# Kernel optimization log

Measured on AMD Instinct MI355X. Metric: run time of the kernel, lower is better.

The kernel has to match this reference:

```python
import jax, jax.numpy as jnp
import numpy as np

B = 131072
INPUT_DIM = 256
HIDDEN_DIM = 512
LATENT_DIM = 64
K = 5


def setup_inputs() -> dict:
    key = jax.random.key(0)
    ks = jax.random.split(key, 12)

    def lin(k, out_d, in_d):
        kw, kb = jax.random.split(k)
        bound = 1.0 / np.sqrt(in_d)
        W = jax.random.uniform(kw, (out_d, in_d), jnp.float32, -bound, bound)
        b = jax.random.uniform(kb, (out_d,), jnp.float32, -bound, bound)
        return W, b

    x = jax.random.normal(ks[0], (B, INPUT_DIM), jnp.float32)
    W_eh, b_eh = lin(ks[1], HIDDEN_DIM, INPUT_DIM)      # encoder hidden Linear
    W_eo, b_eo = lin(ks[2], LATENT_DIM, HIDDEN_DIM)     # encoder out Linear
    W_dh, b_dh = lin(ks[3], HIDDEN_DIM, LATENT_DIM)     # decoder hidden Linear
    W_do, b_do = lin(ks[4], INPUT_DIM, HIDDEN_DIM)      # decoder out Linear
    pre_bias = jnp.zeros((INPUT_DIM,), jnp.float32)
    latent_bias = jax.random.uniform(ks[5], (LATENT_DIM,), jnp.float32, -0.1, 0.1)
    decoder_bias = jnp.zeros((INPUT_DIM,), jnp.float32)
    return {
        "x": x, "pre_bias": pre_bias,
        "W_eh": W_eh, "b_eh": b_eh, "W_eo": W_eo, "b_eo": b_eo,
        "latent_bias": latent_bias,
        "W_dh": W_dh, "b_dh": b_dh, "W_do": W_do, "b_do": b_do,
        "decoder_bias": decoder_bias,
    }


def reference(x, pre_bias, W_eh, b_eh, W_eo, b_eo, latent_bias,
              W_dh, b_dh, W_do, b_do, decoder_bias):
    # encode: pre-bias centering -> hidden MLP (relu) -> latent pre-activation
    xc = x - pre_bias                                   # [B, input_dim]
    h = jax.nn.relu(xc @ W_eh.T + b_eh)                 # [B, hidden]
    pre_act = h @ W_eo.T + b_eo + latent_bias           # [B, latent]

    # TopK activation: keep raw top-k values (no ReLU), zero the rest
    vals, idx = jax.lax.top_k(pre_act, K)               # [B, K]
    rows = jnp.arange(pre_act.shape[0])[:, None]        # [B, 1]
    sparse_latent = jnp.zeros_like(pre_act).at[rows, idx].set(vals)
    mask = jnp.zeros(pre_act.shape, jnp.bool_).at[rows, idx].set(True)

    # decode: hidden MLP (relu) -> output linear + decoder_bias + pre_bias
    hd = jax.nn.relu(sparse_latent @ W_dh.T + b_dh)     # [B, hidden]
    recon = hd @ W_do.T + b_do + decoder_bias + pre_bias  # [B, input_dim]

    sparsity = mask.astype(jnp.float32).mean()
    return recon, sparse_latent, pre_act, mask, sparsity
```

## Files before the change

kernel.cpp:

```cpp
#include <hip/hip_runtime.h>
#include <hip/hip_bf16.h>
#include <stdint.h>

#define B_TOT 131072
#define GAP_TAU 2.5e-4f

typedef short v8s __attribute__((ext_vector_type(8)));
typedef float v4f __attribute__((ext_vector_type(4)));

__device__ __forceinline__ unsigned short f2bf(float f) {
    union { __hip_bfloat16 b; unsigned short s; } v;
    v.b = __float2bfloat16(f);
    return v.s;
}
__device__ __forceinline__ float bf2f(unsigned short s) {
    union { unsigned u; float f; } v; v.u = ((unsigned)s) << 16;
    return v.f;
}
__device__ __forceinline__ unsigned pack2(float lo, float hi) {
    return (unsigned)f2bf(lo) | ((unsigned)f2bf(hi) << 16);
}

__global__ void k_prep(const float* __restrict__ W_dh,
                       const float* __restrict__ b_do,
                       const float* __restrict__ dec_b,
                       const float* __restrict__ pre_bias,
                       const float* __restrict__ W_do,
                       const float* __restrict__ W_eh,
                       const float* __restrict__ W_eo,
                       unsigned short* __restrict__ WdhB,
                       float* __restrict__ bias3,
                       unsigned short* __restrict__ Wdo_frag,
                       unsigned short* __restrict__ WehHi,
                       unsigned short* __restrict__ WehLo,
                       unsigned short* __restrict__ WeoHi,
                       unsigned short* __restrict__ WeoLo,
                       float* __restrict__ WehT,
                       float* __restrict__ WeoT,
                       float* __restrict__ spars_out,
                       int* __restrict__ fcount)
{
    int t = blockIdx.x * blockDim.x + threadIdx.x;
    int nthr = gridDim.x * blockDim.x;
    for (int g = t; g < 32 * 2 * 64; g += nthr) {
        int lane = g & 63;
        int rem = g >> 6;
        int kc = rem & 1, ht = rem >> 1;
        int h = ht * 16 + (lane & 15);
        int l = kc * 32 + (lane >> 4) * 8;
        const float* src = &W_dh[(size_t)h * 64 + l];
        unsigned short* dst = &WdhB[(size_t)g * 8];
        #pragma unroll
        for (int i = 0; i < 8; i++) dst[i] = f2bf(src[i]);
    }
    for (int g = t; g < 16384; g += nthr) {
        int lane = g & 63;
        int q = g >> 6;
        int nt = q >> 4, kc = q & 15;
        int col = nt * 16 + (lane & 15);
        int kbase = kc * 32 + (lane >> 4) * 8;
        const float* src = &W_do[(size_t)col * 512 + kbase];
        unsigned short* dst = &Wdo_frag[(size_t)g * 8];
        #pragma unroll
        for (int i = 0; i < 8; i++) dst[i] = f2bf(src[i]);
    }
    for (int g = t; g < 32 * 8 * 64; g += nthr) {
        int lane = g & 63;
        int rem = g >> 6;
        int kcg = rem & 7, ct = rem >> 3;
        int c = ct * 16 + (lane & 15);
        int k = kcg * 32 + (lane >> 4) * 8;
        const float* src = &W_eh[(size_t)c * 256 + k];
        #pragma unroll
        for (int i = 0; i < 8; i++) {
            unsigned short hi = f2bf(src[i]);
            WehHi[(size_t)g * 8 + i] = hi;
            WehLo[(size_t)g * 8 + i] = f2bf(src[i] - bf2f(hi));
        }
    }
    for (int g = t; g < 4 * 16 * 64; g += nthr) {
        int lane = g & 63;
        int rem = g >> 6;
        int kcg = rem & 15, lt = rem >> 4;
        int l = lt * 16 + (lane & 15);
        int k = kcg * 32 + (lane >> 4) * 8;
        const float* src = &W_eo[(size_t)l * 512 + k];
        #pragma unroll
        for (int i = 0; i < 8; i++) {
            unsigned short hi = f2bf(src[i]);
            WeoHi[(size_t)g * 8 + i] = hi;
            WeoLo[(size_t)g * 8 + i] = f2bf(src[i] - bf2f(hi));
        }
    }
    for (int i = t; i < 256 * 512; i += nthr) {
        int k = i >> 9, j = i & 511;
        WehT[i] = W_eh[(size_t)j * 256 + k];
    }
    for (int i = t; i < 512 * 64; i += nthr) {
        int k = i >> 6, l = i & 63;
        WeoT[i] = W_eo[(size_t)l * 512 + k];
    }
    if (t < 256) bias3[t] = b_do[t] + dec_b[t] + pre_bias[t];
    if (t == 0) { spars_out[0] = 5.0f / 64.0f; *fcount = 0; }
}


__global__ __launch_bounds__(512, 4)
void k_enc1(const float* __restrict__ x,
            const float* __restrict__ pre_bias,
            const unsigned short* __restrict__ WehHi,
            const unsigned short* __restrict__ WehLo,
            const float* __restrict__ b_eh,
            unsigned short* __restrict__ hHi,
            unsigned short* __restrict__ hLo)
{
    __shared__ __align__(16) unsigned short aH[64 * 256];
    __shared__ __align__(16) unsigned short aL[64 * 256];
    const int t    = threadIdx.x;
    const int lane = t & 63;
    const int w    = t >> 6;
    const int rb   = blockIdx.x * 64;

    #pragma unroll
    for (int i = 0; i < 4; i++) {
        const int f    = t + i * 512;
        const int srow = f >> 5;
        const int kc   = (f >> 2) & 7;
        const int skq  = f & 3;
        const float* xp = &x[(size_t)(rb + srow) * 256 + kc * 32 + skq * 8];
        const float* pp = &pre_bias[kc * 32 + skq * 8];
        const float4 v0 = *reinterpret_cast<const float4*>(xp);
        const float4 v1 = *reinterpret_cast<const float4*>(xp + 4);
        const float4 p0 = *reinterpret_cast<const float4*>(pp);
        const float4 p1 = *reinterpret_cast<const float4*>(pp + 4);
        float fv[8] = {v0.x - p0.x, v0.y - p0.y, v0.z - p0.z, v0.w - p0.w,
                       v1.x - p1.x, v1.y - p1.y, v1.z - p1.z, v1.w - p1.w};
        unsigned hi2[4], lo2[4];
        #pragma unroll
        for (int q = 0; q < 4; q++) {
            unsigned short h0 = f2bf(fv[q * 2]), h1 = f2bf(fv[q * 2 + 1]);
            hi2[q] = (unsigned)h0 | ((unsigned)h1 << 16);
            lo2[q] = pack2(fv[q * 2] - bf2f(h0), fv[q * 2 + 1] - bf2f(h1));
        }
        const int off = srow * 512 + ((kc * 64 + skq * 16) ^ ((srow & 7) << 4));
        *reinterpret_cast<uint4*>((char*)aH + off) = *reinterpret_cast<uint4*>(hi2);
        *reinterpret_cast<uint4*>((char*)aL + off) = *reinterpret_cast<uint4*>(lo2);
    }
    __syncthreads();

    const int rt0 = rb >> 4;
    const int q   = lane >> 4;

    #pragma unroll 1
    for (int pass = 0; pass < 2; ++pass) {
        const int ct0 = w * 4 + pass * 2;

        v4f acc[4][2];
        #pragma unroll
        for (int i = 0; i < 4; i++)
            #pragma unroll
            for (int j = 0; j < 2; j++) acc[i][j] = (v4f){0.f, 0.f, 0.f, 0.f};

        #pragma unroll 4
        for (int kc = 0; kc < 8; ++kc) {
            v8s wh[2], wl[2];
            #pragma unroll
            for (int ntl = 0; ntl < 2; ntl++) {
                const size_t idx = ((size_t)((ct0 + ntl) * 8 + kc) * 64 + lane) * 8;
                wh[ntl] = *reinterpret_cast<const v8s*>(&WehHi[idx]);
                wl[ntl] = *reinterpret_cast<const v8s*>(&WehLo[idx]);
            }
            v8s ah[4], al[4];
            #pragma unroll
            for (int mt = 0; mt < 4; mt++) {
                const int row = mt * 16 + (lane & 15);
                const int off = row * 512 + ((kc * 64 + (lane >> 4) * 16) ^ ((row & 7) << 4));
                ah[mt] = *reinterpret_cast<const v8s*>((const char*)aH + off);
                al[mt] = *reinterpret_cast<const v8s*>((const char*)aL + off);
            }
            #pragma unroll
            for (int mt = 0; mt < 4; mt++) {
                #pragma unroll
                for (int ntl = 0; ntl < 2; ntl++) {
                    acc[mt][ntl] = __builtin_amdgcn_mfma_f32_16x16x32_bf16(wh[ntl], ah[mt], acc[mt][ntl], 0, 0, 0);
                    acc[mt][ntl] = __builtin_amdgcn_mfma_f32_16x16x32_bf16(wl[ntl], ah[mt], acc[mt][ntl], 0, 0, 0);
                    acc[mt][ntl] = __builtin_amdgcn_mfma_f32_16x16x32_bf16(wh[ntl], al[mt], acc[mt][ntl], 0, 0, 0);
                }
            }
        }
        #pragma unroll
        for (int mt = 0; mt < 4; mt++) {
            #pragma unroll
            for (int ntl = 0; ntl < 2; ntl++) {
                const int ct = ct0 + ntl;
                const int c  = ct * 16 + q * 4;
                const float4 be = *reinterpret_cast<const float4*>(&b_eh[c]);
                float h0 = fmaxf(acc[mt][ntl][0] + be.x, 0.f);
                float h1 = fmaxf(acc[mt][ntl][1] + be.y, 0.f);
                float h2 = fmaxf(acc[mt][ntl][2] + be.z, 0.f);
                float h3 = fmaxf(acc[mt][ntl][3] + be.w, 0.f);
                unsigned short s0 = f2bf(h0), s1 = f2bf(h1), s2 = f2bf(h2), s3 = f2bf(h3);
                uint2 phi = { (unsigned)s0 | ((unsigned)s1 << 16), (unsigned)s2 | ((unsigned)s3 << 16) };
                uint2 plo = { pack2(h0 - bf2f(s0), h1 - bf2f(s1)),
                              pack2(h2 - bf2f(s2), h3 - bf2f(s3)) };
                const int oct = ct * 2 + (q >> 1);
                const size_t base = (((size_t)(rt0 + mt) * 64 + oct) * 16 + (lane & 15)) * 8 + (q & 1) * 4;
                *reinterpret_cast<uint2*>(&hHi[base]) = phi;
                *reinterpret_cast<uint2*>(&hLo[base]) = plo;
            }
        }
    }
}

__global__ __launch_bounds__(256, 4)
void k_enc2_topk(const unsigned short* __restrict__ hHi,
                 const unsigned short* __restrict__ hLo,
                 const unsigned short* __restrict__ WeoHi,
                 const unsigned short* __restrict__ WeoLo,
                 const float* __restrict__ b_eo,
                 const float* __restrict__ lat_b,
                 float* __restrict__ pre_out,
                 float* __restrict__ mask_out,
                 float* __restrict__ sl_out,
                 int*   __restrict__ fcount,
                 int*   __restrict__ flist)
{
    __shared__ float pa[128][68];
    __shared__ unsigned long long mbits[128];
    const int t    = threadIdx.x;
    const int lane = t & 63;
    const int w    = t >> 6;
    const int rb   = blockIdx.x * 128;
    const int rtA  = (rb >> 4) + w * 2;
    const int rtB  = rtA + 1;

    v4f acc[2][4];
    #pragma unroll
    for (int s = 0; s < 2; s++)
        #pragma unroll
        for (int i = 0; i < 4; i++) acc[s][i] = (v4f){0.f, 0.f, 0.f, 0.f};

    #pragma unroll 2
    for (int kcl = 0; kcl < 16; ++kcl) {
        const size_t baseA = ((size_t)(rtA * 64 + kcl * 4 + (lane >> 4)) * 16 + (lane & 15)) * 8;
        const size_t baseB = ((size_t)(rtB * 64 + kcl * 4 + (lane >> 4)) * 16 + (lane & 15)) * 8;
        const v8s hhA = *reinterpret_cast<const v8s*>(&hHi[baseA]);
        const v8s hlA = *reinterpret_cast<const v8s*>(&hLo[baseA]);
        const v8s hhB = *reinterpret_cast<const v8s*>(&hHi[baseB]);
        const v8s hlB = *reinterpret_cast<const v8s*>(&hLo[baseB]);
        #pragma unroll
        for (int lt = 0; lt < 4; lt++) {
            const size_t idx = ((size_t)(lt * 16 + kcl) * 64 + lane) * 8;
            const v8s wh = *reinterpret_cast<const v8s*>(&WeoHi[idx]);
            const v8s wl = *reinterpret_cast<const v8s*>(&WeoLo[idx]);
            acc[0][lt] = __builtin_amdgcn_mfma_f32_16x16x32_bf16(wh, hhA, acc[0][lt], 0, 0, 0);
            acc[0][lt] = __builtin_amdgcn_mfma_f32_16x16x32_bf16(wl, hhA, acc[0][lt], 0, 0, 0);
            acc[0][lt] = __builtin_amdgcn_mfma_f32_16x16x32_bf16(wh, hlA, acc[0][lt], 0, 0, 0);
            acc[1][lt] = __builtin_amdgcn_mfma_f32_16x16x32_bf16(wh, hhB, acc[1][lt], 0, 0, 0);
            acc[1][lt] = __builtin_amdgcn_mfma_f32_16x16x32_bf16(wl, hhB, acc[1][lt], 0, 0, 0);
            acc[1][lt] = __builtin_amdgcn_mfma_f32_16x16x32_bf16(wh, hlB, acc[1][lt], 0, 0, 0);
        }
    }
    #pragma unroll
    for (int s = 0; s < 2; s++) {
        const int row = w * 32 + s * 16 + (lane & 15);
        #pragma unroll
        for (int lt = 0; lt < 4; lt++) {
            const int l0 = lt * 16 + ((lane >> 4) << 2);
            const float4 be = *reinterpret_cast<const float4*>(&b_eo[l0]);
            const float4 lb = *reinterpret_cast<const float4*>(&lat_b[l0]);
            float4 o;
            o.x = acc[s][lt][0] + be.x + lb.x;
            o.y = acc[s][lt][1] + be.y + lb.y;
            o.z = acc[s][lt][2] + be.z + lb.z;
            o.w = acc[s][lt][3] + be.w + lb.w;
            *reinterpret_cast<float4*>(&pa[row][l0]) = o;
        }
    }
    __syncthreads();
    if (t < 128) {
        int r = t;
        unsigned long long used = 0ULL;
        float bv[5];
        #pragma unroll
        for (int p = 0; p < 5; p++) {
            float best = -3.402823466e38f; int bidx = 0;
            for (int j = 0; j < 64; j++) {
                float v = pa[r][j];
                if (!((used >> j) & 1ULL) && v > best) { best = v; bidx = j; }
            }
            used |= 1ULL << bidx;
            bv[p] = best;
        }
        mbits[r] = used;
        float v6 = -3.402823466e38f;
        for (int j = 0; j < 64; j++) {
            float v = pa[r][j];
            if (!((used >> j) & 1ULL) && v > v6) v6 = v;
        }
        if (bv[4] - v6 < GAP_TAU) {
            int slot = atomicAdd(fcount, 1);
            flist[slot] = rb + r;
        }
    }
    __syncthreads();
    {
        const int c = (t & 15) * 4;
        #pragma unroll
        for (int pass = 0; pass < 8; pass++) {
            const int row = pass * 16 + (t >> 4);
            const size_t gr = (size_t)(rb + row);
            const unsigned long long bits = mbits[row];
            const float p0 = pa[row][c + 0], p1 = pa[row][c + 1];
            const float p2 = pa[row][c + 2], p3 = pa[row][c + 3];
            const float m0 = (float)((bits >> (c + 0)) & 1ULL);
            const float m1 = (float)((bits >> (c + 1)) & 1ULL);
            const float m2 = (float)((bits >> (c + 2)) & 1ULL);
            const float m3 = (float)((bits >> (c + 3)) & 1ULL);
            float4 pv = {p0, p1, p2, p3};
            float4 mv = {m0, m1, m2, m3};
            float4 sv = {m0 * p0, m1 * p1, m2 * p2, m3 * p3};
            *reinterpret_cast<float4*>(&pre_out[gr * 64 + c])  = pv;
            *reinterpret_cast<float4*>(&mask_out[gr * 64 + c]) = mv;
            *reinterpret_cast<float4*>(&sl_out[gr * 64 + c])   = sv;
        }
    }
}

__global__ __launch_bounds__(256)
void k_repair(const float* __restrict__ x,
              const float* __restrict__ pre_bias,
              const float* __restrict__ WehT,
              const float* __restrict__ b_eh,
              const float* __restrict__ WeoT,
              const float* __restrict__ b_eo,
              const float* __restrict__ lat_b,
              const int* __restrict__ fcount,
              const int* __restrict__ flist,
              float* __restrict__ pre_out,
              float* __restrict__ mask_out,
              float* __restrict__ sl_out)
{
    __shared__ float xs[256];
    __shared__ float hs[512];
    __shared__ float part[64][4];
    const int t = threadIdx.x;
    const int n = *fcount;
    #pragma unroll 1
    for (int it = blockIdx.x; it < n; it += gridDim.x) {
        const int r = flist[it];
        xs[t] = x[(size_t)r * 256 + t] - pre_bias[t];
        __syncthreads();
        {
            float a0 = 0.f, a1 = 0.f;
            #pragma unroll 8
            for (int k = 0; k < 256; ++k) {
                const float xk = xs[k];
                a0 = fmaf(WehT[(size_t)k * 512 + t], xk, a0);
                a1 = fmaf(WehT[(size_t)k * 512 + t + 256], xk, a1);
            }
            hs[t]       = fmaxf(a0 + b_eh[t], 0.f);
            hs[t + 256] = fmaxf(a1 + b_eh[t + 256], 0.f);
        }
        __syncthreads();
        {
            const int l = t & 63, q = t >> 6;
            float acc = 0.f;
            const int k0 = q * 128;
            #pragma unroll 8
            for (int k = k0; k < k0 + 128; ++k)
                acc = fmaf(WeoT[(size_t)k * 64 + l], hs[k], acc);
            part[l][q] = acc;
        }
        __syncthreads();
        if (t < 64) {
            const float v = ((part[t][0] + part[t][1]) + (part[t][2] + part[t][3]))
                            + b_eo[t] + lat_b[t];
            unsigned long long used = 0ULL;
            #pragma unroll
            for (int p = 0; p < 5; p++) {
                float cand = ((used >> t) & 1ULL) ? -3.402823466e38f : v;
                float m = cand;
                #pragma unroll
                for (int off = 1; off < 64; off <<= 1)
                    m = fmaxf(m, __shfl_xor(m, off));
                const unsigned long long msk = __ballot(cand == m);
                const int idx = __ffsll((long long)msk) - 1;
                used |= 1ULL << idx;
            }
            const size_t gr = (size_t)r;
            const float mb = (float)((used >> t) & 1ULL);
            pre_out[gr * 64 + t]  = v;
            mask_out[gr * 64 + t] = mb;
            sl_out[gr * 64 + t]   = mb * v;
        }
        __syncthreads();
    }
}

__device__ __forceinline__ void hd_phase1(unsigned short* __restrict__ buf,
                                          const unsigned short* __restrict__ slA,
                                          const unsigned short* __restrict__ WdhB,
                                          const float* __restrict__ b_dh,
                                          int c, int w, int lane)
{
    v4f ah[2][4];
    #pragma unroll
    for (int htl = 0; htl < 2; htl++) {
        const int h0 = (c * 8 + w * 2 + htl) * 16 + ((lane >> 4) << 2);
        const float4 bd = *reinterpret_cast<const float4*>(&b_dh[h0]);
        #pragma unroll
        for (int mt = 0; mt < 4; mt++) ah[htl][mt] = (v4f){bd.x, bd.y, bd.z, bd.w};
    }
    #pragma unroll
    for (int kc = 0; kc < 2; kc++) {
        v8s sa[4];
        #pragma unroll
        for (int mt = 0; mt < 4; mt++)
            sa[mt] = *reinterpret_cast<const v8s*>(&slA[((kc * 4 + mt) * 64 + lane) * 8]);
        #pragma unroll
        for (int htl = 0; htl < 2; htl++) {
            const int ht = c * 8 + w * 2 + htl;
            const v8s wb = *reinterpret_cast<const v8s*>(&WdhB[((size_t)(ht * 2 + kc) * 64 + lane) * 8]);
            #pragma unroll
            for (int mt = 0; mt < 4; mt++)
                ah[htl][mt] = __builtin_amdgcn_mfma_f32_16x16x32_bf16(wb, sa[mt], ah[htl][mt], 0, 0, 0);
        }
    }
    #pragma unroll
    for (int htl = 0; htl < 2; htl++) {
        const int hbase = (w * 2 + htl) * 16 + ((lane >> 4) << 2);
        const int kcgl  = hbase >> 5;
        const int lp    = (((hbase & 31) >> 3) << 4) + (lane & 15);
        const int ii    = hbase & 7;
        #pragma unroll
        for (int mt = 0; mt < 4; mt++) {
            uint2 o;
            o.x = pack2(fmaxf(ah[htl][mt][0], 0.f), fmaxf(ah[htl][mt][1], 0.f));
            o.y = pack2(fmaxf(ah[htl][mt][2], 0.f), fmaxf(ah[htl][mt][3], 0.f));
            *reinterpret_cast<uint2*>(&buf[((kcgl * 4 + mt) * 64 + lp) * 8 + ii]) = o;
        }
    }
}

__global__ __launch_bounds__(256)
void k_dec(const float* __restrict__ sl,
           const float* __restrict__ b_dh,
           const unsigned short* __restrict__ WdhB,
           const unsigned short* __restrict__ Wdo_frag,
           const float* __restrict__ bias3,
           float* __restrict__ recon)
{
    __shared__ __align__(16) unsigned short slA[2 * 4 * 64 * 8];
    __shared__ __align__(16) unsigned short hdA[2][4 * 4 * 64 * 8];
    const int t    = threadIdx.x;
    const int rb   = blockIdx.x * 64;
    const int lane = t & 63;
    const int w    = t >> 6;

    {
        const int row = t >> 2;
        const int seg = (t & 3) * 16;
        const float* sp = &sl[(size_t)(rb + row) * 64 + seg];
        const int mt = row >> 4;
        #pragma unroll
        for (int q = 0; q < 4; q++) {
            const float4 v = *reinterpret_cast<const float4*>(sp + q * 4);
            const float vals[4] = {v.x, v.y, v.z, v.w};
            #pragma unroll
            for (int e = 0; e < 4; e++) {
                const int k  = seg + q * 4 + e;
                const int kc = k >> 5;
                const int lp = ((k & 31) >> 3) * 16 + (row & 15);
                slA[((kc * 4 + mt) * 64 + lp) * 8 + (k & 7)] = f2bf(vals[e]);
            }
        }
    }
    __syncthreads();

    const int g  = w >> 1;
    const int ch = w & 1;

    v4f accM[2][8];
    #pragma unroll
    for (int s = 0; s < 2; s++)
        #pragma unroll
        for (int n = 0; n < 8; n++) accM[s][n] = (v4f){0.f, 0.f, 0.f, 0.f};

    hd_phase1(hdA[0], slA, WdhB, b_dh, 0, w, lane);
    __syncthreads();

    #pragma unroll 1
    for (int c = 0; c < 4; ++c) {
        if (c < 3)
            hd_phase1(hdA[(c + 1) & 1], slA, WdhB, b_dh, c + 1, w, lane);
        const unsigned short* buf = hdA[c & 1];
        #pragma unroll
        for (int kcgl = 0; kcgl < 4; ++kcgl) {
            const int kcg = c * 4 + kcgl;
            const v8s af0 = *reinterpret_cast<const v8s*>(&buf[((kcgl * 4 + g * 2 + 0) * 64 + lane) * 8]);
            const v8s af1 = *reinterpret_cast<const v8s*>(&buf[((kcgl * 4 + g * 2 + 1) * 64 + lane) * 8]);
            #pragma unroll
            for (int ntl = 0; ntl < 8; ntl++) {
                const int ntg = ch * 8 + ntl;
                const v8s bf = *reinterpret_cast<const v8s*>(
                    Wdo_frag + ((size_t)(ntg * 16 + kcg) * 64 + lane) * 8);
                accM[0][ntl] = __builtin_amdgcn_mfma_f32_16x16x32_bf16(af0, bf, accM[0][ntl], 0, 0, 0);
                accM[1][ntl] = __builtin_amdgcn_mfma_f32_16x16x32_bf16(af1, bf, accM[1][ntl], 0, 0, 0);
            }
        }
        __syncthreads();
    }
    #pragma unroll
    for (int s = 0; s < 2; s++) {
        const int rowbase = rb + (g * 2 + s) * 16;
        #pragma unroll
        for (int ntl = 0; ntl < 8; ntl++) {
            const int col = ch * 128 + ntl * 16 + (lane & 15);
            const float bz = bias3[col];
            #pragma unroll
            for (int j = 0; j < 4; j++) {
                const size_t row = (size_t)(rowbase + (lane >> 4) * 4 + j);
                recon[row * 256 + col] = accM[s][ntl][j] + bz;
            }
        }
    }
}

extern "C" void kernel_launch(void* const* d_in, const int* in_sizes, int n_in,
                              void* d_out, int out_size, void* d_ws, size_t ws_size,
                              hipStream_t stream)
{
    const float* x        = (const float*)d_in[0];
    const float* pre_bias = (const float*)d_in[1];
    const float* W_eh     = (const float*)d_in[2];
    const float* b_eh     = (const float*)d_in[3];
    const float* W_eo     = (const float*)d_in[4];
    const float* b_eo     = (const float*)d_in[5];
    const float* lat_b    = (const float*)d_in[6];
    const float* W_dh     = (const float*)d_in[7];
    const float* b_dh     = (const float*)d_in[8];
    const float* W_do     = (const float*)d_in[9];
    const float* b_do     = (const float*)d_in[10];
    const float* dec_b    = (const float*)d_in[11];

    float* out = (float*)d_out;
    float* recon_out = out;
    float* sl_out    = out + (size_t)B_TOT * 256;
    float* pre_out   = sl_out + (size_t)B_TOT * 64;
    float* mask_out  = pre_out + (size_t)B_TOT * 64;
    float* spars_out = mask_out + (size_t)B_TOT * 64;

    char* ws = (char*)d_ws;
    unsigned short* WdhB  = (unsigned short*)ws;
    float* bias3          = (float*)(ws + 131072);
    unsigned short* WdoF  = (unsigned short*)(ws + 132096);
    unsigned short* WehHi = (unsigned short*)(ws + 394240);
    unsigned short* WehLo = (unsigned short*)(ws + 656384);
    unsigned short* WeoHi = (unsigned short*)(ws + 918528);
    unsigned short* WeoLo = (unsigned short*)(ws + 984064);
    int* fcount           = (int*)(ws + 1049600);
    int* flist            = (int*)(ws + 1049664);
    float* WehT           = (float*)(ws + 1573952);
    float* WeoT           = (float*)(ws + 2098240);
    unsigned short* hHi   = (unsigned short*)(ws + 2229312);
    unsigned short* hLo   = hHi + (size_t)B_TOT * 512;

    k_prep<<<32, 256, 0, stream>>>(W_dh, b_do, dec_b, pre_bias, W_do, W_eh, W_eo,
                                   WdhB, bias3, WdoF, WehHi, WehLo, WeoHi, WeoLo,
                                   WehT, WeoT, spars_out, fcount);

    k_enc1<<<B_TOT / 64, 512, 0, stream>>>(x, pre_bias, WehHi, WehLo, b_eh, hHi, hLo);

    k_enc2_topk<<<B_TOT / 128, 256, 0, stream>>>(hHi, hLo, WeoHi, WeoLo, b_eo, lat_b,
                                                 pre_out, mask_out, sl_out,
                                                 fcount, flist);

    k_repair<<<256, 256, 0, stream>>>(x, pre_bias, WehT, b_eh, WeoT, b_eo, lat_b,
                                      fcount, flist, pre_out, mask_out, sl_out);

    k_dec<<<B_TOT / 64, 256, 0, stream>>>(sl_out, b_dh, WdhB, WdoF, bias3, recon_out);
}
```

Before: 404.1 us.

## Fuse decoder into enc2/top-k kernel and recompute repaired rows in repair kernel

The decoder MLP is merged into the encoder-2/top-k kernel. Each block now decodes its 128 rows straight from the shared-memory pre-activations and mask bits, so the sparse latent no longer has to be read back from global memory and one kernel launch disappears. Because the repair kernel runs after decoding, it now recomputes the decoder in fp32 for the flagged rows, using a new transposed W_do copy built in prep. Shared memory per block grows and the launch bound drops to 2 blocks per CU, which may lower occupancy.

```diff
diff --git a/kernel.cpp b/kernel.cpp
--- a/kernel.cpp
+++ b/kernel.cpp
@@ -37,6 +37,7 @@
                        unsigned short* __restrict__ WeoLo,
                        float* __restrict__ WehT,
                        float* __restrict__ WeoT,
+                       float* __restrict__ WdoT,
                        float* __restrict__ spars_out,
                        int* __restrict__ fcount)
 {
@@ -99,6 +100,10 @@
     for (int i = t; i < 512 * 64; i += nthr) {
         int k = i >> 6, l = i & 63;
         WeoT[i] = W_eo[(size_t)l * 512 + k];
+    }
+    for (int i = t; i < 512 * 256; i += nthr) {
+        int h = i >> 8, c = i & 255;
+        WdoT[i] = W_do[(size_t)c * 512 + h];
     }
     if (t < 256) bias3[t] = b_do[t] + dec_b[t] + pre_bias[t];
     if (t == 0) { spars_out[0] = 5.0f / 64.0f; *fcount = 0; }
@@ -212,21 +217,73 @@
     }
 }
 
-__global__ __launch_bounds__(256, 4)
-void k_enc2_topk(const unsigned short* __restrict__ hHi,
-                 const unsigned short* __restrict__ hLo,
-                 const unsigned short* __restrict__ WeoHi,
-                 const unsigned short* __restrict__ WeoLo,
-                 const float* __restrict__ b_eo,
-                 const float* __restrict__ lat_b,
-                 float* __restrict__ pre_out,
-                 float* __restrict__ mask_out,
-                 float* __restrict__ sl_out,
-                 int*   __restrict__ fcount,
-                 int*   __restrict__ flist)
+__device__ __forceinline__ void hd_phase1(unsigned short* __restrict__ buf,
+                                          const unsigned short* __restrict__ slA,
+                                          const unsigned short* __restrict__ WdhB,
+                                          const float* __restrict__ b_dh,
+                                          int c, int w, int lane)
+{
+    v4f ah[2][4];
+    #pragma unroll
+    for (int htl = 0; htl < 2; htl++) {
+        const int h0 = (c * 8 + w * 2 + htl) * 16 + ((lane >> 4) << 2);
+        const float4 bd = *reinterpret_cast<const float4*>(&b_dh[h0]);
+        #pragma unroll
+        for (int mt = 0; mt < 4; mt++) ah[htl][mt] = (v4f){bd.x, bd.y, bd.z, bd.w};
+    }
+    #pragma unroll
+    for (int kc = 0; kc < 2; kc++) {
+        v8s sa[4];
+        #pragma unroll
+        for (int mt = 0; mt < 4; mt++)
+            sa[mt] = *reinterpret_cast<const v8s*>(&slA[((kc * 4 + mt) * 64 + lane) * 8]);
+        #pragma unroll
+        for (int htl = 0; htl < 2; htl++) {
+            const int ht = c * 8 + w * 2 + htl;
+            const v8s wb = *reinterpret_cast<const v8s*>(&WdhB[((size_t)(ht * 2 + kc) * 64 + lane) * 8]);
+            #pragma unroll
+            for (int mt = 0; mt < 4; mt++)
+                ah[htl][mt] = __builtin_amdgcn_mfma_f32_16x16x32_bf16(wb, sa[mt], ah[htl][mt], 0, 0, 0);
+        }
+    }
+    #pragma unroll
+    for (int htl = 0; htl < 2; htl++) {
+        const int hbase = (w * 2 + htl) * 16 + ((lane >> 4) << 2);
+        const int kcgl  = hbase >> 5;
+        const int lp    = (((hbase & 31) >> 3) << 4) + (lane & 15);
+        const int ii    = hbase & 7;
+        #pragma unroll
+        for (int mt = 0; mt < 4; mt++) {
+            uint2 o;
+            o.x = pack2(fmaxf(ah[htl][mt][0], 0.f), fmaxf(ah[htl][mt][1], 0.f));
+            o.y = pack2(fmaxf(ah[htl][mt][2], 0.f), fmaxf(ah[htl][mt][3], 0.f));
+            *reinterpret_cast<uint2*>(&buf[((kcgl * 4 + mt) * 64 + lp) * 8 + ii]) = o;
+        }
+    }
+}
+
+__global__ __launch_bounds__(256, 2)
+void k_enc2dec(const unsigned short* __restrict__ hHi,
+               const unsigned short* __restrict__ hLo,
+               const unsigned short* __restrict__ WeoHi,
+               const unsigned short* __restrict__ WeoLo,
+               const float* __restrict__ b_eo,
+               const float* __restrict__ lat_b,
+               float* __restrict__ pre_out,
+               float* __restrict__ mask_out,
+               float* __restrict__ sl_out,
+               int*   __restrict__ fcount,
+               int*   __restrict__ flist,
+               const float* __restrict__ b_dh,
+               const unsigned short* __restrict__ WdhB,
+               const unsigned short* __restrict__ Wdo_frag,
+               const float* __restrict__ bias3,
+               float* __restrict__ recon)
 {
     __shared__ float pa[128][68];
     __shared__ unsigned long long mbits[128];
+    __shared__ __align__(16) unsigned short slA[2 * 4 * 64 * 8];
+    __shared__ __align__(16) unsigned short hdA[2][4 * 4 * 64 * 8];
     const int t    = threadIdx.x;
     const int lane = t & 63;
     const int w    = t >> 6;
@@ -234,47 +291,49 @@
     const int rtA  = (rb >> 4) + w * 2;
     const int rtB  = rtA + 1;
 
-    v4f acc[2][4];
-    #pragma unroll
-    for (int s = 0; s < 2; s++)
-        #pragma unroll
-        for (int i = 0; i < 4; i++) acc[s][i] = (v4f){0.f, 0.f, 0.f, 0.f};
-
-    #pragma unroll 2
-    for (int kcl = 0; kcl < 16; ++kcl) {
-        const size_t baseA = ((size_t)(rtA * 64 + kcl * 4 + (lane >> 4)) * 16 + (lane & 15)) * 8;
-        const size_t baseB = ((size_t)(rtB * 64 + kcl * 4 + (lane >> 4)) * 16 + (lane & 15)) * 8;
-        const v8s hhA = *reinterpret_cast<const v8s*>(&hHi[baseA]);
-        const v8s hlA = *reinterpret_cast<const v8s*>(&hLo[baseA]);
-        const v8s hhB = *reinterpret_cast<const v8s*>(&hHi[baseB]);
-        const v8s hlB = *reinterpret_cast<const v8s*>(&hLo[baseB]);
-        #pragma unroll
-        for (int lt = 0; lt < 4; lt++) {
-            const size_t idx = ((size_t)(lt * 16 + kcl) * 64 + lane) * 8;
-            const v8s wh = *reinterpret_cast<const v8s*>(&WeoHi[idx]);
-            const v8s wl = *reinterpret_cast<const v8s*>(&WeoLo[idx]);
-            acc[0][lt] = __builtin_amdgcn_mfma_f32_16x16x32_bf16(wh, hhA, acc[0][lt], 0, 0, 0);
-            acc[0][lt] = __builtin_amdgcn_mfma_f32_16x16x32_bf16(wl, hhA, acc[0][lt], 0, 0, 0);
-            acc[0][lt] = __builtin_amdgcn_mfma_f32_16x16x32_bf16(wh, hlA, acc[0][lt], 0, 0, 0);
-            acc[1][lt] = __builtin_amdgcn_mfma_f32_16x16x32_bf16(wh, hhB, acc[1][lt], 0, 0, 0);
-            acc[1][lt] = __builtin_amdgcn_mfma_f32_16x16x32_bf16(wl, hhB, acc[1][lt], 0, 0, 0);
-            acc[1][lt] = __builtin_amdgcn_mfma_f32_16x16x32_bf16(wh, hlB, acc[1][lt], 0, 0, 0);
-        }
-    }
-    #pragma unroll
-    for (int s = 0; s < 2; s++) {
-        const int row = w * 32 + s * 16 + (lane & 15);
-        #pragma unroll
-        for (int lt = 0; lt < 4; lt++) {
-            const int l0 = lt * 16 + ((lane >> 4) << 2);
-            const float4 be = *reinterpret_cast<const float4*>(&b_eo[l0]);
-            const float4 lb = *reinterpret_cast<const float4*>(&lat_b[l0]);
-            float4 o;
-            o.x = acc[s][lt][0] + be.x + lb.x;
-            o.y = acc[s][lt][1] + be.y + lb.y;
-            o.z = acc[s][lt][2] + be.z + lb.z;
-            o.w = acc[s][lt][3] + be.w + lb.w;
-            *reinterpret_cast<float4*>(&pa[row][l0]) = o;
+    {
+        v4f acc[2][4];
+        #pragma unroll
+        for (int s = 0; s < 2; s++)
+            #pragma unroll
+            for (int i = 0; i < 4; i++) acc[s][i] = (v4f){0.f, 0.f, 0.f, 0.f};
+
+        #pragma unroll 2
+        for (int kcl = 0; kcl < 16; ++kcl) {
+            const size_t baseA = ((size_t)(rtA * 64 + kcl * 4 + (lane >> 4)) * 16 + (lane & 15)) * 8;
+            const size_t baseB = ((size_t)(rtB * 64 + kcl * 4 + (lane >> 4)) * 16 + (lane & 15)) * 8;
+            const v8s hhA = *reinterpret_cast<const v8s*>(&hHi[baseA]);
+            const v8s hlA = *reinterpret_cast<const v8s*>(&hLo[baseA]);
+            const v8s hhB = *reinterpret_cast<const v8s*>(&hHi[baseB]);
+            const v8s hlB = *reinterpret_cast<const v8s*>(&hLo[baseB]);
+            #pragma unroll
+            for (int lt = 0; lt < 4; lt++) {
+                const size_t idx = ((size_t)(lt * 16 + kcl) * 64 + lane) * 8;
+                const v8s wh = *reinterpret_cast<const v8s*>(&WeoHi[idx]);
+                const v8s wl = *reinterpret_cast<const v8s*>(&WeoLo[idx]);
+                acc[0][lt] = __builtin_amdgcn_mfma_f32_16x16x32_bf16(wh, hhA, acc[0][lt], 0, 0, 0);
+                acc[0][lt] = __builtin_amdgcn_mfma_f32_16x16x32_bf16(wl, hhA, acc[0][lt], 0, 0, 0);
+                acc[0][lt] = __builtin_amdgcn_mfma_f32_16x16x32_bf16(wh, hlA, acc[0][lt], 0, 0, 0);
+                acc[1][lt] = __builtin_amdgcn_mfma_f32_16x16x32_bf16(wh, hhB, acc[1][lt], 0, 0, 0);
+                acc[1][lt] = __builtin_amdgcn_mfma_f32_16x16x32_bf16(wl, hhB, acc[1][lt], 0, 0, 0);
+                acc[1][lt] = __builtin_amdgcn_mfma_f32_16x16x32_bf16(wh, hlB, acc[1][lt], 0, 0, 0);
+            }
+        }
+        #pragma unroll
+        for (int s = 0; s < 2; s++) {
+            const int row = w * 32 + s * 16 + (lane & 15);
+            #pragma unroll
+            for (int lt = 0; lt < 4; lt++) {
+                const int l0 = lt * 16 + ((lane >> 4) << 2);
+                const float4 be = *reinterpret_cast<const float4*>(&b_eo[l0]);
+                const float4 lb = *reinterpret_cast<const float4*>(&lat_b[l0]);
+                float4 o;
+                o.x = acc[s][lt][0] + be.x + lb.x;
+                o.y = acc[s][lt][1] + be.y + lb.y;
+                o.z = acc[s][lt][2] + be.z + lb.z;
+                o.w = acc[s][lt][3] + be.w + lb.w;
+                *reinterpret_cast<float4*>(&pa[row][l0]) = o;
+            }
         }
     }
     __syncthreads();
@@ -325,6 +384,79 @@
             *reinterpret_cast<float4*>(&sl_out[gr * 64 + c])   = sv;
         }
     }
+    __syncthreads();
+
+    const int g  = w >> 1;
+    const int ch = w & 1;
+    #pragma unroll 1
+    for (int sb = 0; sb < 2; ++sb) {
+        {
+            const int row  = t >> 2;
+            const int prow = sb * 64 + row;
+            const int seg  = (t & 3) * 16;
+            const unsigned long long bits = mbits[prow];
+            const int mt = row >> 4;
+            #pragma unroll
+            for (int q = 0; q < 4; q++) {
+                const float4 v = *reinterpret_cast<const float4*>(&pa[prow][seg + q * 4]);
+                const float vals[4] = {v.x, v.y, v.z, v.w};
+                #pragma unroll
+                for (int e = 0; e < 4; e++) {
+                    const int k  = seg + q * 4 + e;
+                    const float m = (float)((bits >> k) & 1ULL);
+                    const int kc = k >> 5;
+                    const int lp = ((k & 31) >> 3) * 16 + (row & 15);
+                    slA[((kc * 4 + mt) * 64 + lp) * 8 + (k & 7)] = f2bf(m * vals[e]);
+                }
+            }
+        }
+        __syncthreads();
+
+        v4f accM[2][8];
+        #pragma unroll
+        for (int s = 0; s < 2; s++)
+            #pragma unroll
+            for (int n = 0; n < 8; n++) accM[s][n] = (v4f){0.f, 0.f, 0.f, 0.f};
+
+        hd_phase1(hdA[0], slA, WdhB, b_dh, 0, w, lane);
+        __syncthreads();
+
+        #pragma unroll 1
+        for (int c = 0; c < 4; ++c) {
+            if (c < 3)
+                hd_phase1(hdA[(c + 1) & 1], slA, WdhB, b_dh, c + 1, w, lane);
+            const unsigned short* buf = hdA[c & 1];
+            #pragma unroll
+            for (int kcgl = 0; kcgl < 4; ++kcgl) {
+                const int kcg = c * 4 + kcgl;
+                const v8s af0 = *reinterpret_cast<const v8s*>(&buf[((kcgl * 4 + g * 2 + 0) * 64 + lane) * 8]);
+                const v8s af1 = *reinterpret_cast<const v8s*>(&buf[((kcgl * 4 + g * 2 + 1) * 64 + lane) * 8]);
+                #pragma unroll
+                for (int ntl = 0; ntl < 8; ntl++) {
+                    const int ntg = ch * 8 + ntl;
+                    const v8s bf = *reinterpret_cast<const v8s*>(
+                        Wdo_frag + ((size_t)(ntg * 16 + kcg) * 64 + lane) * 8);
+                    accM[0][ntl] = __builtin_amdgcn_mfma_f32_16x16x32_bf16(af0, bf, accM[0][ntl], 0, 0, 0);
+                    accM[1][ntl] = __builtin_amdgcn_mfma_f32_16x16x32_bf16(af1, bf, accM[1][ntl], 0, 0, 0);
+                }
+            }
+            __syncthreads();
+        }
+        #pragma unroll
+        for (int s = 0; s < 2; s++) {
+            const int rowbase = rb + sb * 64 + (g * 2 + s) * 16;
+            #pragma unroll
+            for (int ntl = 0; ntl < 8; ntl++) {
+                const int col = ch * 128 + ntl * 16 + (lane & 15);
+                const float bz = bias3[col];
+                #pragma unroll
+                for (int j = 0; j < 4; j++) {
+                    const size_t row = (size_t)(rowbase + (lane >> 4) * 4 + j);
+                    recon[row * 256 + col] = accM[s][ntl][j] + bz;
+                }
+            }
+        }
+    }
 }
 
 __global__ __launch_bounds__(256)
@@ -339,11 +471,17 @@
               const int* __restrict__ flist,
               float* __restrict__ pre_out,
               float* __restrict__ mask_out,
-              float* __restrict__ sl_out)
+              float* __restrict__ sl_out,
+              const float* __restrict__ W_dh,
+              const float* __restrict__ b_dh,
+              const float* __restrict__ WdoT,
+              const float* __restrict__ bias3,
+              float* __restrict__ recon)
 {
     __shared__ float xs[256];
     __shared__ float hs[512];
     __shared__ float part[64][4];
+    __shared__ float msv[64];
     const int t = threadIdx.x;
     const int n = *fcount;
     #pragma unroll 1
@@ -393,137 +531,30 @@
             pre_out[gr * 64 + t]  = v;
             mask_out[gr * 64 + t] = mb;
             sl_out[gr * 64 + t]   = mb * v;
-        }
-        __syncthreads();
-    }
-}
-
-__device__ __forceinline__ void hd_phase1(unsigned short* __restrict__ buf,
-                                          const unsigned short* __restrict__ slA,
-                                          const unsigned short* __restrict__ WdhB,
-                                          const float* __restrict__ b_dh,
-                                          int c, int w, int lane)
-{
-    v4f ah[2][4];
-    #pragma unroll
-    for (int htl = 0; htl < 2; htl++) {
-        const int h0 = (c * 8 + w * 2 + htl) * 16 + ((lane >> 4) << 2);
-        const float4 bd = *reinterpret_cast<const float4*>(&b_dh[h0]);
-        #pragma unroll
-        for (int mt = 0; mt < 4; mt++) ah[htl][mt] = (v4f){bd.x, bd.y, bd.z, bd.w};
-    }
-    #pragma unroll
-    for (int kc = 0; kc < 2; kc++) {
-        v8s sa[4];
-        #pragma unroll
-        for (int mt = 0; mt < 4; mt++)
-            sa[mt] = *reinterpret_cast<const v8s*>(&slA[((kc * 4 + mt) * 64 + lane) * 8]);
-        #pragma unroll
-        for (int htl = 0; htl < 2; htl++) {
-            const int ht = c * 8 + w * 2 + htl;
-            const v8s wb = *reinterpret_cast<const v8s*>(&WdhB[((size_t)(ht * 2 + kc) * 64 + lane) * 8]);
-            #pragma unroll
-            for (int mt = 0; mt < 4; mt++)
-                ah[htl][mt] = __builtin_amdgcn_mfma_f32_16x16x32_bf16(wb, sa[mt], ah[htl][mt], 0, 0, 0);
-        }
-    }
-    #pragma unroll
-    for (int htl = 0; htl < 2; htl++) {
-        const int hbase = (w * 2 + htl) * 16 + ((lane >> 4) << 2);
-        const int kcgl  = hbase >> 5;
-        const int lp    = (((hbase & 31) >> 3) << 4) + (lane & 15);
-        const int ii    = hbase & 7;
-        #pragma unroll
-        for (int mt = 0; mt < 4; mt++) {
-            uint2 o;
-            o.x = pack2(fmaxf(ah[htl][mt][0], 0.f), fmaxf(ah[htl][mt][1], 0.f));
-            o.y = pack2(fmaxf(ah[htl][mt][2], 0.f), fmaxf(ah[htl][mt][3], 0.f));
-            *reinterpret_cast<uint2*>(&buf[((kcgl * 4 + mt) * 64 + lp) * 8 + ii]) = o;
-        }
-    }
-}
-
-__global__ __launch_bounds__(256)
-void k_dec(const float* __restrict__ sl,
-           const float* __restrict__ b_dh,
-           const unsigned short* __restrict__ WdhB,
-           const unsigned short* __restrict__ Wdo_frag,
-           const float* __restrict__ bias3,
-           float* __restrict__ recon)
-{
-    __shared__ __align__(16) unsigned short slA[2 * 4 * 64 * 8];
-    __shared__ __align__(16) unsigned short hdA[2][4 * 4 * 64 * 8];
-    const int t    = threadIdx.x;
-    const int rb   = blockIdx.x * 64;
-    const int lane = t & 63;
-    const int w    = t >> 6;
-
-    {
-        const int row = t >> 2;
-        const int seg = (t & 3) * 16;
-        const float* sp = &sl[(size_t)(rb + row) * 64 + seg];
-        const int mt = row >> 4;
-        #pragma unroll
-        for (int q = 0; q < 4; q++) {
-            const float4 v = *reinterpret_cast<const float4*>(sp + q * 4);
-            const float vals[4] = {v.x, v.y, v.z, v.w};
-            #pragma unroll
-            for (int e = 0; e < 4; e++) {
-                const int k  = seg + q * 4 + e;
-                const int kc = k >> 5;
-                const int lp = ((k & 31) >> 3) * 16 + (row & 15);
-                slA[((kc * 4 + mt) * 64 + lp) * 8 + (k & 7)] = f2bf(vals[e]);
-            }
-        }
-    }
-    __syncthreads();
-
-    const int g  = w >> 1;
-    const int ch = w & 1;
-
-    v4f accM[2][8];
-    #pragma unroll
-    for (int s = 0; s < 2; s++)
-        #pragma unroll
-        for (int n = 0; n < 8; n++) accM[s][n] = (v4f){0.f, 0.f, 0.f, 0.f};
-
-    hd_phase1(hdA[0], slA, WdhB, b_dh, 0, w, lane);
-    __syncthreads();
-
-    #pragma unroll 1
-    for (int c = 0; c < 4; ++c) {
-        if (c < 3)
-            hd_phase1(hdA[(c + 1) & 1], slA, WdhB, b_dh, c + 1, w, lane);
-        const unsigned short* buf = hdA[c & 1];
-        #pragma unroll
-        for (int kcgl = 0; kcgl < 4; ++kcgl) {
-            const int kcg = c * 4 + kcgl;
-            const v8s af0 = *reinterpret_cast<const v8s*>(&buf[((kcgl * 4 + g * 2 + 0) * 64 + lane) * 8]);
-            const v8s af1 = *reinterpret_cast<const v8s*>(&buf[((kcgl * 4 + g * 2 + 1) * 64 + lane) * 8]);
-            #pragma unroll
-            for (int ntl = 0; ntl < 8; ntl++) {
-                const int ntg = ch * 8 + ntl;
-                const v8s bf = *reinterpret_cast<const v8s*>(
-                    Wdo_frag + ((size_t)(ntg * 16 + kcg) * 64 + lane) * 8);
-                accM[0][ntl] = __builtin_amdgcn_mfma_f32_16x16x32_bf16(af0, bf, accM[0][ntl], 0, 0, 0);
-                accM[1][ntl] = __builtin_amdgcn_mfma_f32_16x16x32_bf16(af1, bf, accM[1][ntl], 0, 0, 0);
-            }
-        }
-        __syncthreads();
-    }
-    #pragma unroll
-    for (int s = 0; s < 2; s++) {
-        const int rowbase = rb + (g * 2 + s) * 16;
-        #pragma unroll
-        for (int ntl = 0; ntl < 8; ntl++) {
-            const int col = ch * 128 + ntl * 16 + (lane & 15);
-            const float bz = bias3[col];
-            #pragma unroll
-            for (int j = 0; j < 4; j++) {
-                const size_t row = (size_t)(rowbase + (lane >> 4) * 4 + j);
-                recon[row * 256 + col] = accM[s][ntl][j] + bz;
-            }
-        }
+            msv[t] = mb * v;
+        }
+        __syncthreads();
+        {
+            float a0 = b_dh[t], a1 = b_dh[t + 256];
+            #pragma unroll 8
+            for (int j = 0; j < 64; ++j) {
+                const float s = msv[j];
+                a0 = fmaf(s, W_dh[(size_t)t * 64 + j], a0);
+                a1 = fmaf(s, W_dh[(size_t)(t + 256) * 64 + j], a1);
+            }
+            __syncthreads();
+            hs[t]       = fmaxf(a0, 0.f);
+            hs[t + 256] = fmaxf(a1, 0.f);
+        }
+        __syncthreads();
+        {
+            float a = bias3[t];
+            #pragma unroll 8
+            for (int h = 0; h < 512; ++h)
+                a = fmaf(hs[h], WdoT[(size_t)h * 256 + t], a);
+            recon[(size_t)r * 256 + t] = a;
+        }
+        __syncthreads();
     }
 }
 
@@ -563,21 +594,22 @@
     int* flist            = (int*)(ws + 1049664);
     float* WehT           = (float*)(ws + 1573952);
     float* WeoT           = (float*)(ws + 2098240);
-    unsigned short* hHi   = (unsigned short*)(ws + 2229312);
+    float* WdoT           = (float*)(ws + 2229312);
+    unsigned short* hHi   = (unsigned short*)(ws + 2753600);
     unsigned short* hLo   = hHi + (size_t)B_TOT * 512;
 
     k_prep<<<32, 256, 0, stream>>>(W_dh, b_do, dec_b, pre_bias, W_do, W_eh, W_eo,
                                    WdhB, bias3, WdoF, WehHi, WehLo, WeoHi, WeoLo,
-                                   WehT, WeoT, spars_out, fcount);
+                                   WehT, WeoT, WdoT, spars_out, fcount);
 
     k_enc1<<<B_TOT / 64, 512, 0, stream>>>(x, pre_bias, WehHi, WehLo, b_eh, hHi, hLo);
 
-    k_enc2_topk<<<B_TOT / 128, 256, 0, stream>>>(hHi, hLo, WeoHi, WeoLo, b_eo, lat_b,
-                                                 pre_out, mask_out, sl_out,
-                                                 fcount, flist);
+    k_enc2dec<<<B_TOT / 128, 256, 0, stream>>>(hHi, hLo, WeoHi, WeoLo, b_eo, lat_b,
+                                               pre_out, mask_out, sl_out,
+                                               fcount, flist,
+                                               b_dh, WdhB, WdoF, bias3, recon_out);
 
     k_repair<<<256, 256, 0, stream>>>(x, pre_bias, WehT, b_eh, WeoT, b_eo, lat_b,
-                                      fcount, flist, pre_out, mask_out, sl_out);
-
-    k_dec<<<B_TOT / 64, 256, 0, stream>>>(sl_out, b_dh, WdhB, WdoF, bias3, recon_out);
-}
+                                      fcount, flist, pre_out, mask_out, sl_out,
+                                      W_dh, b_dh, WdoT, bias3, recon_out);
+}
```

Result: slower. 510.1 us (+26.2%).
